# Kernel optimization log

Hardware: AMD Instinct MI355X
Metric: run time of the kernel (lower is better)

Reference implementation:

```python
import jax, jax.numpy as jnp
import numpy as np

FEATURE_SIZE = 128
STRIDE = 16
BASE_SIZE = 16
RATIOS = [0.5, 1, 2]
SCALES = [8, 16, 32]


def _generate_anchors(feature_size, stride):
    # Faithful to the torch module's numpy anchor generation (incl. rounding).
    size = BASE_SIZE * BASE_SIZE
    size_ratios = size / np.array(RATIOS)
    ws = np.round(np.sqrt(size_ratios))
    hs = np.round(ws * np.array(RATIOS))
    base = []
    for w, h in zip(ws, hs):
        for s in SCALES:
            base.append([0.0, 0.0, w * s, h * s])
    base = np.array(base)  # [9, 4]
    xo, yo = np.meshgrid(np.arange(feature_size), np.arange(feature_size), indexing='ij')
    # original loop order: x outer, y inner, then 9 base anchors
    centers = np.stack([xo * stride, yo * stride], axis=-1).reshape(-1, 1, 2)  # [F*F,1,2]
    wh = np.broadcast_to(base[None, :, 2:4], (feature_size * feature_size, 9, 2))
    anchors = np.concatenate([np.broadcast_to(centers, wh.shape), wh], axis=-1).reshape(-1, 4)
    return jnp.asarray(anchors, dtype=jnp.float32)  # [F*F*9, 4]


def _conv(x, w, b, pad):
    y = jax.lax.conv_general_dilated(
        x, w, window_strides=(1, 1), padding=[(pad, pad), (pad, pad)],
        dimension_numbers=('NCHW', 'OIHW', 'NCHW'))
    return y + b[None, :, None, None]


def setup_inputs() -> dict:
    key = jax.random.key(0)
    ks = jax.random.split(key, 4)
    F = FEATURE_SIZE
    x = jax.random.normal(ks[0], (1, 1024, F, F), dtype=jnp.float32)
    base_w = jax.random.normal(ks[1], (512, 1024, 3, 3), dtype=jnp.float32) * 0.01
    base_b = jnp.zeros((512,), dtype=jnp.float32)
    cls_w = jax.random.normal(ks[2], (18, 512, 1, 1), dtype=jnp.float32) * 0.01
    cls_b = jnp.zeros((18,), dtype=jnp.float32)
    reg_w = jax.random.normal(ks[3], (36, 512, 1, 1), dtype=jnp.float32) * 0.01
    reg_b = jnp.zeros((36,), dtype=jnp.float32)
    return {"x": x, "base_w": base_w, "base_b": base_b,
            "cls_w": cls_w, "cls_b": cls_b, "reg_w": reg_w, "reg_b": reg_b}


def reference(x, base_w, base_b, cls_w, cls_b, reg_w, reg_b):
    F = FEATURE_SIZE
    anchors = _generate_anchors(F, STRIDE)  # [N,4], N = F*F*9

    rpn_conv = jax.nn.relu(_conv(x, base_w, base_b, pad=1))        # [1,512,F,F]
    rpn_cls = _conv(rpn_conv, cls_w, cls_b, pad=0)                  # [1,18,F,F]
    # softmax over the 2-way fg/bg axis after reshape, as in the original
    cls_rs = rpn_cls.reshape(1, 2, 9 * F, F)
    cls_prob = jax.nn.softmax(cls_rs, axis=1).reshape(1, 18, F, F)
    rpn_reg = _conv(rpn_conv, reg_w, reg_b, pad=0)                  # [1,36,F,F]

    cls = jnp.transpose(cls_prob, (0, 2, 3, 1)).reshape(-1, 2)      # [N,2]
    reg = jnp.transpose(rpn_reg, (0, 2, 3, 1)).reshape(-1, 4)       # [N,4]

    # Vectorized decode — faithful to the original per-anchor loop math:
    # p0 = ax + aw*d0 ; p1 = ay + ah*d1 ; p2 = aw + exp(d2) ; p3 = ah + exp(d3)
    p0 = anchors[:, 0] + anchors[:, 2] * reg[:, 0]
    p1 = anchors[:, 1] + anchors[:, 3] * reg[:, 1]
    p2 = anchors[:, 2] + jnp.exp(reg[:, 2])
    p3 = anchors[:, 3] + jnp.exp(reg[:, 3])
    proposals = jnp.stack([p0, p1, p2, p3], axis=-1)                # [N,4]
    scores = cls[:, 1]                                              # [N]
    return jnp.concatenate([proposals, scores[:, None]], axis=-1)   # [N,5]
```

## Files before the change

kernel.cpp:

```cpp
#include <hip/hip_runtime.h>
#include <hip/hip_bf16.h>

typedef unsigned short u16;
typedef short s8v __attribute__((ext_vector_type(8)));
typedef float f4v __attribute__((ext_vector_type(4)));

#define F 128
#define CIN 1024
#define CMID 512
#define XP 130
#define K9 9216

#define A_ELEMS 8704
#define B_ELEMS 8192
#define AOFF(b) ((b) * A_ELEMS)
#define BOFF(b) (2 * A_ELEMS + (b) * B_ELEMS)

__device__ __forceinline__ u16 f2bf(float v) {
    union { float f; unsigned u; } x; x.f = v;
    unsigned r = x.u + 0x7fff + ((x.u >> 16) & 1);
    return (u16)(r >> 16);
}
__device__ __forceinline__ float bf2f(u16 u) {
    union { unsigned u; float f; } x; x.u = ((unsigned)u) << 16; return x.f;
}

__device__ __forceinline__ void gl16(const u16* g, u16* l) {
    __builtin_amdgcn_global_load_lds(
        (const __attribute__((address_space(1))) void*)g,
        (__attribute__((address_space(3))) void*)l,
        16, 0, 0);
}

__constant__ float WBASE[9] = {184.f, 368.f, 736.f, 128.f, 256.f, 512.f,  88.f, 176.f, 352.f};
__constant__ float HBASE[9] = { 96.f, 192.f, 384.f, 128.f, 256.f, 512.f, 176.f, 352.f, 704.f};

__global__ __launch_bounds__(256) void prep_all(
    const float* __restrict__ x, const float* __restrict__ bw,
    const float* __restrict__ cls_w, const float* __restrict__ reg_w,
    u16* __restrict__ xpad, u16* __restrict__ wt, u16* __restrict__ wc) {
    __shared__ char ldsraw[128 * 65 * 4];
    const int b = blockIdx.x;
    const int tid = threadIdx.x;

    if (b < 512) {
        float (*lds)[65] = (float(*)[65])ldsraw;
        const int h  = b >> 2;
        const int c0 = (b & 3) * 256;
        #pragma unroll 1
        for (int cc = 0; cc < 4; ++cc) {
            const int cb = c0 + cc * 64;
            {
                const int w4 = (tid & 31) * 4;
                const int cl = tid >> 5;
                #pragma unroll
                for (int p = 0; p < 8; ++p) {
                    const int c = p * 8 + cl;
                    f4v v = *(const f4v*)&x[(cb + c) * (F * F) + h * F + w4];
                    #pragma unroll
                    for (int k = 0; k < 4; ++k) lds[w4 + k][c] = v[k];
                }
            }
            __syncthreads();
            {
                const int cs = (tid & 7) * 8;
                const int wb = tid >> 3;
                #pragma unroll
                for (int p = 0; p < 4; ++p) {
                    const int w = p * 32 + wb;
                    s8v v;
                    #pragma unroll
                    for (int j = 0; j < 8; ++j) v[j] = (short)f2bf(lds[w][cs + j]);
                    *(s8v*)&xpad[((h + 1) * XP + (w + 1)) * CIN + cb + cs] = v;
                }
            }
            __syncthreads();
        }
    } else if (b < 1024) {
        u16* lds = (u16*)ldsraw;
        const int oc = b - 512;
        for (int k = 0; k < 36; ++k) {
            int idx = k * 256 + tid;
            float v = bw[oc * K9 + idx];
            int c = idx / 9, q = idx - c * 9;
            lds[q * 1033 + c] = f2bf(v);
        }
        __syncthreads();
        for (int k = 0; k < 36; ++k) {
            int idx = k * 256 + tid;
            int q = idx >> 10, c = idx & 1023;
            wt[oc * K9 + idx] = lds[q * 1033 + c];
        }
    } else if (b < 1282) {
        int t = (b - 1024) * 256 + tid;
        int cell = t >> 7, c8 = (t & 127) * 8;
        int h, w;
        if (cell < 130)      { h = 0;   w = cell; }
        else if (cell < 260) { h = 129; w = cell - 130; }
        else { int rm = cell - 260; h = 1 + (rm >> 1); w = (rm & 1) * 129; }
        s8v z = {};
        *(s8v*)&xpad[(h * XP + w) * CIN + c8] = z;
    } else {
        int t = (b - 1282) * 256 + tid;
        int oc = t >> 9, c = t & 511;
        float v = 0.f;
        if (oc < 18)      v = cls_w[oc * 512 + c];
        else if (oc < 54) v = reg_w[(oc - 18) * 512 + c];
        wc[t] = f2bf(v);
    }
}

__global__ __launch_bounds__(256, 2) void gemm_conv(
    const u16* __restrict__ xpad, const u16* __restrict__ wt,
    const float* __restrict__ bias, u16* __restrict__ rpn) {
    __shared__ u16 smem[2 * A_ELEMS + 2 * B_ELEMS];
    const int tid = threadIdx.x;
    const int w_id = (blockIdx.x & 7) * 64 + (blockIdx.x >> 3);
    const int oc0 = ((w_id & 7) >> 1) * 128;
    const int gh  = (w_id >> 3) * 2 + (w_id & 1);

    const int lane = tid & 63;
    const int wv = tid >> 6;
    const int lm = lane & 15;
    const int lq = lane >> 4;
    const int wm = (wv >> 1) * 64;
    const int wn = (wv & 1) * 64;

    const int sw = (lane & 7) ^ ((lane >> 3) & 7);
    const u16* pA = xpad + (lane >> 3) * CIN + sw * 8;
    const u16* pB = wt + (size_t)(oc0 + wv * 32 + (lane >> 3)) * K9 + sw * 8;

    f4v acc[4][4] = {};

    auto issueA = [&](int ms) {
        const int dy = ms >> 4, cc = ms & 15;
        const u16* src = pA + ((gh + dy) * XP) * CIN + cc * 64;
        u16* dst = &smem[AOFF(ms & 1)];
        #pragma unroll
        for (int jj = 0; jj < 4; ++jj) {
            const int ci = wv * 4 + jj;
            gl16(src + ci * 8 * CIN, dst + ci * 512);
        }
        if (wv == 0) gl16(src + 16 * 8 * CIN, dst + 16 * 512);
    };
    auto issueB = [&](int ms, int dx, int buf) {
        const int dy = ms >> 4, cc = ms & 15;
        const int dydx = dy * 3 + dx;
        const u16* src = pB + dydx * CIN + cc * 64;
        u16* dst = &smem[BOFF(buf) + wv * 32 * 64];
        #pragma unroll
        for (int jj = 0; jj < 4; ++jj)
            gl16(src + jj * 8 * K9, dst + jj * 8 * 64);
    };

    issueA(0);
    issueB(0, 0, 0);
    __syncthreads();

    int t = 0;
    for (int ms = 0; ms < 48; ++ms) {
        const u16* Ab = &smem[AOFF(ms & 1)];
        #pragma unroll
        for (int dx = 0; dx < 3; ++dx, ++t) {
            if (t + 1 < 144) {
                const int msn = (dx == 2) ? ms + 1 : ms;
                const int dxn = (dx == 2) ? 0 : dx + 1;
                issueB(msn, dxn, (t + 1) & 1);
            }
            if (dx == 0 && ms + 1 < 48) issueA(ms + 1);
            const u16* Bb = &smem[BOFF(t & 1)];
            #pragma unroll
            for (int kk = 0; kk < 2; ++kk) {
                const int kseg = kk * 4 + lq;
                s8v af[4], bfr[4];
                #pragma unroll
                for (int i = 0; i < 4; ++i) {
                    const int ra = wm + i * 16 + lm + dx;
                    const int rb = wn + i * 16 + lm;
                    af[i]  = *(const s8v*)&Ab[ra * 64 + ((kseg ^ (ra & 7)) << 3)];
                    bfr[i] = *(const s8v*)&Bb[rb * 64 + ((kseg ^ (rb & 7)) << 3)];
                }
                #pragma unroll
                for (int mi = 0; mi < 4; ++mi)
                    #pragma unroll
                    for (int ni = 0; ni < 4; ++ni)
                        acc[mi][ni] = __builtin_amdgcn_mfma_f32_16x16x32_bf16(
                            af[mi], bfr[ni], acc[mi][ni], 0, 0, 0);
            }
            __syncthreads();
        }
    }

    #pragma unroll
    for (int ni = 0; ni < 4; ++ni) {
        const int oc = oc0 + wn + ni * 16 + lm;
        const float bv = bias[oc];
        #pragma unroll
        for (int mi = 0; mi < 4; ++mi) {
            #pragma unroll
            for (int rr = 0; rr < 4; ++rr) {
                const int m = wm + mi * 16 + lq * 4 + rr;
                float v = acc[mi][ni][rr] + bv;
                v = v > 0.f ? v : 0.f;
                rpn[(gh * 128 + m) * CMID + oc] = f2bf(v);
            }
        }
    }
}

__global__ __launch_bounds__(256) void stage23(
    const u16* __restrict__ rpn, const u16* __restrict__ wc,
    const float* __restrict__ cls_b, const float* __restrict__ reg_b,
    float* __restrict__ out) {
    __shared__ float part[4][16][65];
    const int tid = threadIdx.x, lane = tid & 63, wv = tid >> 6;
    const int lm = lane & 15, lq = lane >> 4;
    const int m0 = blockIdx.x * 16;

    f4v acc[4] = {};
    const u16* arow = rpn + (m0 + lm) * CMID + wv * 128 + lq * 8;
    const u16* brow = wc + lm * CMID + wv * 128 + lq * 8;
    #pragma unroll
    for (int k = 0; k < 4; ++k) {
        s8v af = *(const s8v*)(arow + k * 32);
        #pragma unroll
        for (int ni = 0; ni < 4; ++ni) {
            s8v bf = *(const s8v*)(brow + ni * 16 * CMID + k * 32);
            acc[ni] = __builtin_amdgcn_mfma_f32_16x16x32_bf16(af, bf, acc[ni], 0, 0, 0);
        }
    }
    #pragma unroll
    for (int ni = 0; ni < 4; ++ni)
        #pragma unroll
        for (int rr = 0; rr < 4; ++rr)
            part[wv][lq * 4 + rr][ni * 16 + lm] = acc[ni][rr];
    __syncthreads();

    float vsum[4];
    const int col = tid & 63, rb = tid >> 6;
    const float bv = col < 18 ? cls_b[col] : (col < 54 ? reg_b[col - 18] : 0.f);
    #pragma unroll
    for (int rr = 0; rr < 4; ++rr) {
        const int row = rb * 4 + rr;
        vsum[rr] = part[0][row][col] + part[1][row][col]
                 + part[2][row][col] + part[3][row][col] + bv;
    }
    __syncthreads();
    #pragma unroll
    for (int rr = 0; rr < 4; ++rr)
        part[0][rb * 4 + rr][col] = vsum[rr];
    __syncthreads();

    if (tid < 144) {
        const int pl = tid / 9, a = tid - pl * 9;
        const float* v = part[0][pl];
        const int ch = 2 * a + 1;
        const int pair = (ch < 9) ? ch + 9 : ch - 9;
        const float score = 1.f / (1.f + expf(v[pair] - v[ch]));
        const float r0 = v[18 + 4 * a], r1 = v[19 + 4 * a];
        const float r2 = v[20 + 4 * a], r3 = v[21 + 4 * a];
        const float wb = WBASE[a], hb = HBASE[a];
        const int p = m0 + pl;
        const int h = p >> 7, w = p & 127;
        float* o = out + (p * 9 + a) * 5;
        o[0] = h * 16.f + wb * r0;
        o[1] = w * 16.f + hb * r1;
        o[2] = wb + expf(r2);
        o[3] = hb + expf(r3);
        o[4] = score;
    }
}

extern "C" void kernel_launch(void* const* d_in, const int* in_sizes, int n_in,
                              void* d_out, int out_size, void* d_ws, size_t ws_size,
                              hipStream_t stream) {
    const float* x      = (const float*)d_in[0];
    const float* base_w = (const float*)d_in[1];
    const float* base_b = (const float*)d_in[2];
    const float* cls_w  = (const float*)d_in[3];
    const float* cls_b  = (const float*)d_in[4];
    const float* reg_w  = (const float*)d_in[5];
    const float* reg_b  = (const float*)d_in[6];
    float* out = (float*)d_out;

    char* ws = (char*)d_ws;
    u16* xpad = (u16*)ws;
    u16* wt   = (u16*)(ws + 34611200);
    u16* wc   = (u16*)(ws + 34611200 + 9437184);
    u16* rpn  = (u16*)(ws + 34611200 + 9437184 + 65536);

    prep_all<<<1410, 256, 0, stream>>>(x, base_w, cls_w, reg_w, xpad, wt, wc);
    gemm_conv<<<512, 256, 0, stream>>>(xpad, wt, base_b, rpn);
    stage23<<<1024, 256, 0, stream>>>(rpn, wc, cls_b, reg_b, out);
}
```

Measured before the change: 260.4 us.

## Restructure prep transpose to bf16 LDS, simplify weight reorder, double stage23 rows

The input transpose now converts to bf16 before writing LDS and uses one 64-channel chunk per block, launching four times as many blocks with a smaller LDS footprint. The base-weight reorder drops the LDS staging and writes directly from per-channel strided reads. stage23 processes 32 pixels per block instead of 16, halving the grid. These target prep-kernel occupancy and LDS traffic, at the cost of uncoalesced weight reads and less parallelism in stage23.

Result: no change. 259.7 us (-0.2%).

```diff
diff --git a/kernel.cpp b/kernel.cpp
--- a/kernel.cpp
+++ b/kernel.cpp
@@ -2,6 +2,7 @@
 #include <hip/hip_bf16.h>
 
 typedef unsigned short u16;
+typedef short s4v __attribute__((ext_vector_type(4)));
 typedef short s8v __attribute__((ext_vector_type(8)));
 typedef float f4v __attribute__((ext_vector_type(4)));
 
@@ -21,9 +22,6 @@
     unsigned r = x.u + 0x7fff + ((x.u >> 16) & 1);
     return (u16)(r >> 16);
 }
-__device__ __forceinline__ float bf2f(u16 u) {
-    union { unsigned u; float f; } x; x.u = ((unsigned)u) << 16; return x.f;
-}
 
 __device__ __forceinline__ void gl16(const u16* g, u16* l) {
     __builtin_amdgcn_global_load_lds(
@@ -39,60 +37,51 @@
     const float* __restrict__ x, const float* __restrict__ bw,
     const float* __restrict__ cls_w, const float* __restrict__ reg_w,
     u16* __restrict__ xpad, u16* __restrict__ wt, u16* __restrict__ wc) {
-    __shared__ char ldsraw[128 * 65 * 4];
+    __shared__ u16 ldsT[64 * 132];
     const int b = blockIdx.x;
     const int tid = threadIdx.x;
 
-    if (b < 512) {
-        float (*lds)[65] = (float(*)[65])ldsraw;
-        const int h  = b >> 2;
-        const int c0 = (b & 3) * 256;
+    if (b < 2048) {
+        const int h  = b >> 4;
+        const int cb = (b & 15) * 64;
+        {
+            const int L = tid & 31, cl = tid >> 5;
+            const int w4 = L * 4;
+            #pragma unroll
+            for (int p = 0; p < 8; ++p) {
+                const int c = p * 8 + cl;
+                f4v v = *(const f4v*)&x[(cb + c) * (F * F) + h * F + w4];
+                s4v pk;
+                #pragma unroll
+                for (int k = 0; k < 4; ++k) pk[k] = (short)f2bf(v[k]);
+                *(s4v*)&ldsT[c * 132 + w4] = pk;
+            }
+        }
+        __syncthreads();
+        {
+            const int cs = (tid & 7) * 8;
+            const int wb = tid >> 3;
+            #pragma unroll
+            for (int p = 0; p < 4; ++p) {
+                const int w = p * 32 + wb;
+                s8v o;
+                #pragma unroll
+                for (int j = 0; j < 8; ++j) o[j] = (short)ldsT[(cs + j) * 132 + w];
+                *(s8v*)&xpad[((h + 1) * XP + (w + 1)) * CIN + cb + cs] = o;
+            }
+        }
+    } else if (b < 2560) {
+        const int oc = b - 2048;
         #pragma unroll 1
-        for (int cc = 0; cc < 4; ++cc) {
-            const int cb = c0 + cc * 64;
-            {
-                const int w4 = (tid & 31) * 4;
-                const int cl = tid >> 5;
-                #pragma unroll
-                for (int p = 0; p < 8; ++p) {
-                    const int c = p * 8 + cl;
-                    f4v v = *(const f4v*)&x[(cb + c) * (F * F) + h * F + w4];
-                    #pragma unroll
-                    for (int k = 0; k < 4; ++k) lds[w4 + k][c] = v[k];
-                }
-            }
-            __syncthreads();
-            {
-                const int cs = (tid & 7) * 8;
-                const int wb = tid >> 3;
-                #pragma unroll
-                for (int p = 0; p < 4; ++p) {
-                    const int w = p * 32 + wb;
-                    s8v v;
-                    #pragma unroll
-                    for (int j = 0; j < 8; ++j) v[j] = (short)f2bf(lds[w][cs + j]);
-                    *(s8v*)&xpad[((h + 1) * XP + (w + 1)) * CIN + cb + cs] = v;
-                }
-            }
-            __syncthreads();
-        }
-    } else if (b < 1024) {
-        u16* lds = (u16*)ldsraw;
-        const int oc = b - 512;
-        for (int k = 0; k < 36; ++k) {
-            int idx = k * 256 + tid;
-            float v = bw[oc * K9 + idx];
-            int c = idx / 9, q = idx - c * 9;
-            lds[q * 1033 + c] = f2bf(v);
-        }
-        __syncthreads();
-        for (int k = 0; k < 36; ++k) {
-            int idx = k * 256 + tid;
-            int q = idx >> 10, c = idx & 1023;
-            wt[oc * K9 + idx] = lds[q * 1033 + c];
-        }
-    } else if (b < 1282) {
-        int t = (b - 1024) * 256 + tid;
+        for (int p = 0; p < 4; ++p) {
+            const int c = p * 256 + tid;
+            const float* src = bw + oc * K9 + c * 9;
+            #pragma unroll
+            for (int q = 0; q < 9; ++q)
+                wt[oc * K9 + q * 1024 + c] = f2bf(src[q]);
+        }
+    } else if (b < 2818) {
+        int t = (b - 2560) * 256 + tid;
         int cell = t >> 7, c8 = (t & 127) * 8;
         int h, w;
         if (cell < 130)      { h = 0;   w = cell; }
@@ -101,7 +90,7 @@
         s8v z = {};
         *(s8v*)&xpad[(h * XP + w) * CIN + c8] = z;
     } else {
-        int t = (b - 1282) * 256 + tid;
+        int t = (b - 2818) * 256 + tid;
         int oc = t >> 9, c = t & 511;
         float v = 0.f;
         if (oc < 18)      v = cls_w[oc * 512 + c];
@@ -212,62 +201,69 @@
     const u16* __restrict__ rpn, const u16* __restrict__ wc,
     const float* __restrict__ cls_b, const float* __restrict__ reg_b,
     float* __restrict__ out) {
-    __shared__ float part[4][16][65];
+    __shared__ float part[4][32][65];
     const int tid = threadIdx.x, lane = tid & 63, wv = tid >> 6;
     const int lm = lane & 15, lq = lane >> 4;
-    const int m0 = blockIdx.x * 16;
-
-    f4v acc[4] = {};
-    const u16* arow = rpn + (m0 + lm) * CMID + wv * 128 + lq * 8;
-    const u16* brow = wc + lm * CMID + wv * 128 + lq * 8;
-    #pragma unroll
-    for (int k = 0; k < 4; ++k) {
-        s8v af = *(const s8v*)(arow + k * 32);
-        #pragma unroll
-        for (int ni = 0; ni < 4; ++ni) {
-            s8v bf = *(const s8v*)(brow + ni * 16 * CMID + k * 32);
-            acc[ni] = __builtin_amdgcn_mfma_f32_16x16x32_bf16(af, bf, acc[ni], 0, 0, 0);
-        }
-    }
-    #pragma unroll
-    for (int ni = 0; ni < 4; ++ni)
-        #pragma unroll
-        for (int rr = 0; rr < 4; ++rr)
-            part[wv][lq * 4 + rr][ni * 16 + lm] = acc[ni][rr];
-    __syncthreads();
-
-    float vsum[4];
+    const int m0 = blockIdx.x * 32;
+
+    #pragma unroll
+    for (int g = 0; g < 2; ++g) {
+        f4v acc[4] = {};
+        const u16* arow = rpn + (m0 + g * 16 + lm) * CMID + wv * 128 + lq * 8;
+        const u16* brow = wc + lm * CMID + wv * 128 + lq * 8;
+        #pragma unroll
+        for (int k = 0; k < 4; ++k) {
+            s8v af = *(const s8v*)(arow + k * 32);
+            #pragma unroll
+            for (int ni = 0; ni < 4; ++ni) {
+                s8v bf = *(const s8v*)(brow + ni * 16 * CMID + k * 32);
+                acc[ni] = __builtin_amdgcn_mfma_f32_16x16x32_bf16(af, bf, acc[ni], 0, 0, 0);
+            }
+        }
+        #pragma unroll
+        for (int ni = 0; ni < 4; ++ni)
+            #pragma unroll
+            for (int rr = 0; rr < 4; ++rr)
+                part[wv][g * 16 + lq * 4 + rr][ni * 16 + lm] = acc[ni][rr];
+    }
+    __syncthreads();
+
+    float vsum[8];
     const int col = tid & 63, rb = tid >> 6;
     const float bv = col < 18 ? cls_b[col] : (col < 54 ? reg_b[col - 18] : 0.f);
     #pragma unroll
-    for (int rr = 0; rr < 4; ++rr) {
-        const int row = rb * 4 + rr;
+    for (int rr = 0; rr < 8; ++rr) {
+        const int row = rb * 8 + rr;
         vsum[rr] = part[0][row][col] + part[1][row][col]
                  + part[2][row][col] + part[3][row][col] + bv;
     }
     __syncthreads();
     #pragma unroll
-    for (int rr = 0; rr < 4; ++rr)
-        part[0][rb * 4 + rr][col] = vsum[rr];
-    __syncthreads();
-
-    if (tid < 144) {
-        const int pl = tid / 9, a = tid - pl * 9;
-        const float* v = part[0][pl];
-        const int ch = 2 * a + 1;
-        const int pair = (ch < 9) ? ch + 9 : ch - 9;
-        const float score = 1.f / (1.f + expf(v[pair] - v[ch]));
-        const float r0 = v[18 + 4 * a], r1 = v[19 + 4 * a];
-        const float r2 = v[20 + 4 * a], r3 = v[21 + 4 * a];
-        const float wb = WBASE[a], hb = HBASE[a];
-        const int p = m0 + pl;
-        const int h = p >> 7, w = p & 127;
-        float* o = out + (p * 9 + a) * 5;
-        o[0] = h * 16.f + wb * r0;
-        o[1] = w * 16.f + hb * r1;
-        o[2] = wb + expf(r2);
-        o[3] = hb + expf(r3);
-        o[4] = score;
+    for (int rr = 0; rr < 8; ++rr)
+        part[0][rb * 8 + rr][col] = vsum[rr];
+    __syncthreads();
+
+    #pragma unroll 1
+    for (int g = 0; g < 2; ++g) {
+        if (tid < 144) {
+            const int pl0 = tid / 9, a = tid - pl0 * 9;
+            const int pl = g * 16 + pl0;
+            const float* v = part[0][pl];
+            const int ch = 2 * a + 1;
+            const int pair = (ch < 9) ? ch + 9 : ch - 9;
+            const float score = 1.f / (1.f + expf(v[pair] - v[ch]));
+            const float r0 = v[18 + 4 * a], r1 = v[19 + 4 * a];
+            const float r2 = v[20 + 4 * a], r3 = v[21 + 4 * a];
+            const float wb = WBASE[a], hb = HBASE[a];
+            const int p = m0 + pl;
+            const int h = p >> 7, w = p & 127;
+            float* o = out + (p * 9 + a) * 5;
+            o[0] = h * 16.f + wb * r0;
+            o[1] = w * 16.f + hb * r1;
+            o[2] = wb + expf(r2);
+            o[3] = hb + expf(r3);
+            o[4] = score;
+        }
     }
 }
 
@@ -289,7 +285,7 @@
     u16* wc   = (u16*)(ws + 34611200 + 9437184);
     u16* rpn  = (u16*)(ws + 34611200 + 9437184 + 65536);
 
-    prep_all<<<1410, 256, 0, stream>>>(x, base_w, cls_w, reg_w, xpad, wt, wc);
+    prep_all<<<2946, 256, 0, stream>>>(x, base_w, cls_w, reg_w, xpad, wt, wc);
     gemm_conv<<<512, 256, 0, stream>>>(xpad, wt, base_b, rpn);
-    stage23<<<1024, 256, 0, stream>>>(rpn, wc, cls_b, reg_b, out);
-}
+    stage23<<<512, 256, 0, stream>>>(rpn, wc, cls_b, reg_b, out);
+}
```
